# Kernel optimization log

Hardware: AMD Instinct MI355X
Metric: run time of the kernel (lower is better)

## Reference

```python
import jax, jax.numpy as jnp
import numpy as np

N, D, H, E, L = 4096, 512, 8, 131072, 2
DH = D // H  # per-head dim


def _layernorm(x, g, b, eps=1e-5):
    mu = x.mean(-1, keepdims=True)
    v = ((x - mu) ** 2).mean(-1, keepdims=True)
    return (x - mu) * jax.lax.rsqrt(v + eps) * g + b


def setup_inputs() -> dict:
    key = jax.random.key(0)
    ks = jax.random.split(key, 8)
    s = np.float32(1.0 / np.sqrt(D))
    return {
        "x": jax.random.normal(ks[0], (N, D), jnp.float32),
        "edge_index": jax.random.randint(ks[1], (2, E), 0, N),
        "edge_attr": jax.random.normal(ks[2], (E, 16), jnp.float32),
        "W_gcn": jax.random.normal(ks[3], (L, D, D), jnp.float32) * s,
        "ln1_g": jnp.ones((L, D), jnp.float32),
        "ln1_b": jnp.zeros((L, D), jnp.float32),
        "Wq": jax.random.normal(ks[4], (L, D, D), jnp.float32) * s,
        "bq": jnp.zeros((L, D), jnp.float32),
        "Wk": jax.random.normal(ks[5], (L, D, D), jnp.float32) * s,
        "bk": jnp.zeros((L, D), jnp.float32),
        "Wv": jax.random.normal(ks[6], (L, D, D), jnp.float32) * s,
        "bv": jnp.zeros((L, D), jnp.float32),
        "Wo": jax.random.normal(ks[7], (L, D, D), jnp.float32) * s,
        "bo": jnp.zeros((L, D), jnp.float32),
        "ln2_g": jnp.ones((L, D), jnp.float32),
        "ln2_b": jnp.zeros((L, D), jnp.float32),
    }


def reference(x, edge_index, edge_attr, W_gcn, ln1_g, ln1_b, Wq, bq, Wk, bk, Wv, bv, Wo, bo, ln2_g, ln2_b):
    src, dst = edge_index[0], edge_index[1]
    # symmetric GCN normalization (add_self_loops=False): deg from scattering 1s at target
    deg = jax.ops.segment_sum(jnp.ones(src.shape[0], x.dtype), dst, num_segments=N)
    dinv = jnp.where(deg > 0, jax.lax.rsqrt(jnp.maximum(deg, 1e-12)), 0.0)
    enorm = (dinv[src] * dinv[dst])[:, None]  # [E,1]
    scale = 1.0 / np.sqrt(D)  # MHA scale = 1/sqrt(D_x), applied to BOTH Q and K
    for i in range(L):
        # GCNConv (no bias): gather - linear - scatter-sum
        h = x @ W_gcn[i]
        h = jax.ops.segment_sum(h[src] * enorm, dst, num_segments=N)
        # PairNorm (scale=1, scale_individually=False)
        c = h - h.mean(0, keepdims=True)
        h = c * jax.lax.rsqrt(1e-5 + (c * c).sum(-1).mean())
        # residual: relu(x) + x
        h = jax.nn.relu(h) + h
        # LayerNorm 1
        h = _layernorm(h, ln1_g[i], ln1_b[i])
        # MultiHeadAttentionBlock (self-attn, B=1) -- faithful raw reshapes of original
        Q = (h @ Wq[i].T + bq[i]) * scale            # [N,D]
        K = (h @ Wk[i].T + bk[i]) * scale            # [N,D]
        V = h @ Wv[i].T + bv[i]                      # [N,D]
        Qr = Q.reshape(H, DH, N).transpose(0, 2, 1)  # view(B*H,d,L).transpose(1,2)
        Kr = K.reshape(H, DH, N)                     # view(B*H,d,L)
        w = jax.nn.softmax(jnp.einsum('hld,hdm->hlm', Qr, Kr), axis=-1)  # [H,N,N]
        Vr = V.reshape(H, DH, N).transpose(0, 2, 1)  # [H,N,d]
        a = jnp.einsum('hlm,hmd->hld', w, Vr).reshape(N, D)
        h = a @ Wo[i].T + bo[i]
        # LayerNorm 2
        x = _layernorm(h, ln2_g[i], ln2_b[i])
    return x
```

## Files before the change

### kernel.cpp

```cpp
#include <hip/hip_runtime.h>


#define NN 4096
#define DD 512
#define HH 8
#define DH 64
#define EE 131072

typedef float f32x2 __attribute__((ext_vector_type(2)));
typedef float f32x4 __attribute__((ext_vector_type(4)));
typedef short short8 __attribute__((ext_vector_type(8)));
typedef unsigned short u16x4 __attribute__((ext_vector_type(4)));
typedef __bf16 bf16x8 __attribute__((ext_vector_type(8)));

static __device__ __forceinline__ unsigned short f2bf(float f) {
  unsigned u = __float_as_uint(f);
  return (unsigned short)((u + 0x7FFFu + ((u >> 16) & 1u)) >> 16);
}
static __device__ __forceinline__ float bf2f(unsigned short s) {
  return __uint_as_float(((unsigned)s) << 16);
}

static __device__ __forceinline__ f32x4 mfma16(short8 a, short8 b, f32x4 c) {
  return __builtin_amdgcn_mfma_f32_16x16x32_bf16(
      __builtin_bit_cast(bf16x8, a), __builtin_bit_cast(bf16x8, b), c, 0, 0, 0);
}

static __device__ __forceinline__ void gload16(const unsigned short* g, unsigned short* l) {
  __builtin_amdgcn_global_load_lds((const __attribute__((address_space(1))) unsigned int*)g,
                                   (__attribute__((address_space(3))) unsigned int*)l, 16, 0, 0);
}

__global__ __launch_bounds__(256) void deg_k(const int* __restrict__ ei, float* __restrict__ deg) {
  int t = blockIdx.x * 256 + threadIdx.x;
  atomicAdd(&deg[ei[EE + t]], 1.0f);
}

__global__ __launch_bounds__(256) void dinv_k(const float* __restrict__ deg, float* __restrict__ dinv) {
  int t = blockIdx.x * 256 + threadIdx.x;
  float dg = deg[t];
  dinv[t] = dg > 0.f ? rsqrtf(fmaxf(dg, 1e-12f)) : 0.f;
}

__global__ __launch_bounds__(256) void scan_k(const float* __restrict__ deg,
                                              int* __restrict__ rowstart,
                                              int* __restrict__ cursor) {
  __shared__ int part[256];
  const int t = threadIdx.x;
  int loc[16];
  int s = 0;
#pragma unroll
  for (int j = 0; j < 16; ++j) {
    loc[j] = s;
    s += (int)deg[t * 16 + j];
  }
  part[t] = s;
  __syncthreads();
  for (int off = 1; off < 256; off <<= 1) {
    int v = (t >= off) ? part[t - off] : 0;
    __syncthreads();
    part[t] += v;
    __syncthreads();
  }
  int base = (t > 0) ? part[t - 1] : 0;
#pragma unroll
  for (int j = 0; j < 16; ++j) {
    int rs = base + loc[j];
    rowstart[t * 16 + j] = rs;
    cursor[t * 16 + j] = rs;
  }
  if (t == 255) rowstart[4096] = part[255];
}

__global__ __launch_bounds__(256) void csr_fill_k(const int* __restrict__ ei,
                                                  const float* __restrict__ dinv,
                                                  int* __restrict__ cursor,
                                                  int* __restrict__ ecol,
                                                  float* __restrict__ ewt) {
  int e = blockIdx.x * 256 + threadIdx.x;
  int s = ei[e], d = ei[EE + e];
  int pos = atomicAdd(&cursor[d], 1);
  ecol[pos] = s;
  ewt[pos] = dinv[s] * dinv[d];
}

__global__ __launch_bounds__(256) void cvt_k(const float* __restrict__ s,
                                             unsigned short* __restrict__ d, int n4) {
  int i = blockIdx.x * 256 + threadIdx.x;
  if (i < n4) {
    f32x4 v = *(const f32x4*)&s[i * 4];
    u16x4 o;
#pragma unroll
    for (int j = 0; j < 4; ++j) o[j] = f2bf(v[j]);
    *(u16x4*)&d[i * 4] = o;
  }
}

__global__ __launch_bounds__(256) void wtr_k(const float* __restrict__ in,
                                             unsigned short* __restrict__ out) {
  __shared__ unsigned short sm[64][72];
  const int k0 = blockIdx.y * 64, j0 = blockIdx.x * 64;
  const int t = threadIdx.x;
  const int r = t >> 2, q = (t & 3) * 16;
  const float* src = in + (size_t)(k0 + r) * 512 + j0 + q;
#pragma unroll
  for (int jj = 0; jj < 16; ++jj) sm[r][q + jj] = f2bf(src[jj]);
  __syncthreads();
  short8 s0, s1;
#pragma unroll
  for (int j = 0; j < 8; ++j) {
    s0[j] = (short)sm[q + j][r];
    s1[j] = (short)sm[q + 8 + j][r];
  }
  *(short8*)&out[(size_t)(j0 + r) * 512 + k0 + q] = s0;
  *(short8*)&out[(size_t)(j0 + r) * 512 + k0 + q + 8] = s1;
}

__global__ __launch_bounds__(256) void gather_k(const unsigned short* __restrict__ hb,
                                                const int* __restrict__ rowstart,
                                                const int* __restrict__ ecol,
                                                const float* __restrict__ ewt,
                                                float* __restrict__ h1) {
  __shared__ int s_col[256];
  __shared__ float s_w[256];
  const int node = blockIdx.x, t = threadIdx.x;
  const int beg = rowstart[node], end = rowstart[node + 1];
  float a0 = 0.f, a1 = 0.f;
  for (int base = beg; base < end; base += 256) {
    int n = min(256, end - base);
    __syncthreads();
    if (t < n) {
      s_col[t] = ecol[base + t];
      s_w[t] = ewt[base + t];
    }
    __syncthreads();
    for (int j = 0; j < n; ++j) {
      int s = s_col[j];
      float en = s_w[j];
      unsigned v = *(const unsigned*)&hb[(size_t)s * DD + 2 * t];
      a0 += en * __uint_as_float(v << 16);
      a1 += en * __uint_as_float(v & 0xFFFF0000u);
    }
  }
  f32x2 acc = {a0, a1};
  *(f32x2*)&h1[(size_t)node * DD + 2 * t] = acc;
}

template <bool HAS_BIAS, bool OUT_BF16>
__global__ __launch_bounds__(256) void gemm_bt_k(const unsigned short* __restrict__ A,
                                                 const unsigned short* __restrict__ B,
                                                 const float* __restrict__ bias, float scale,
                                                 void* __restrict__ Cv, int M, int Nc, int K) {
  __shared__ __align__(16) unsigned short a_sm[2][64][64];
  __shared__ __align__(16) unsigned short b_sm[2][64][64];
  const int tid = threadIdx.x, w = tid >> 6, lane = tid & 63;
  const int g = lane >> 4, c16 = lane & 15;
  const int n0 = blockIdx.x * 64, m0 = blockIdx.y * 64;
  const int wm = (w >> 1) * 32, wn = (w & 1) * 32;
  const int srow = lane >> 3, cg = lane & 7;
  const int swz = ((cg * 16) ^ (srow << 4)) >> 1;
  const unsigned short* ag = A + (size_t)(m0 + w * 8 + srow) * K + swz;
  const unsigned short* bg = B + (size_t)(n0 + w * 8 + srow) * K + swz;
  f32x4 acc[2][2] = {};

  gload16(ag, &a_sm[0][w * 8][0]);
  gload16(ag + (size_t)32 * K, &a_sm[0][w * 8 + 32][0]);
  gload16(bg, &b_sm[0][w * 8][0]);
  gload16(bg + (size_t)32 * K, &b_sm[0][w * 8 + 32][0]);
  __syncthreads();

  const int rx = (c16 & 7) << 4;
  const int NK = K >> 6;
  for (int ks = 0; ks < NK; ++ks) {
    const int cb = ks & 1;
    if (ks < NK - 1) {
      const size_t ko = (size_t)(ks + 1) * 64;
      gload16(ag + ko, &a_sm[cb ^ 1][w * 8][0]);
      gload16(ag + ko + (size_t)32 * K, &a_sm[cb ^ 1][w * 8 + 32][0]);
      gload16(bg + ko, &b_sm[cb ^ 1][w * 8][0]);
      gload16(bg + ko + (size_t)32 * K, &b_sm[cb ^ 1][w * 8 + 32][0]);
    }
#pragma unroll
    for (int kc = 0; kc < 2; ++kc) {
      const int co = (kc * 64 + g * 16) ^ rx;
      short8 af0 = *(const short8*)((const char*)&a_sm[cb][wm + c16][0] + co);
      short8 af1 = *(const short8*)((const char*)&a_sm[cb][wm + 16 + c16][0] + co);
      short8 bf0 = *(const short8*)((const char*)&b_sm[cb][wn + c16][0] + co);
      short8 bf1 = *(const short8*)((const char*)&b_sm[cb][wn + 16 + c16][0] + co);
      acc[0][0] = mfma16(af0, bf0, acc[0][0]);
      acc[0][1] = mfma16(af0, bf1, acc[0][1]);
      acc[1][0] = mfma16(af1, bf0, acc[1][0]);
      acc[1][1] = mfma16(af1, bf1, acc[1][1]);
    }
    __syncthreads();
  }
#pragma unroll
  for (int fm = 0; fm < 2; ++fm)
#pragma unroll
    for (int fn = 0; fn < 2; ++fn)
#pragma unroll
      for (int r = 0; r < 4; ++r) {
        int row = m0 + wm + fm * 16 + g * 4 + r;
        int col = n0 + wn + fn * 16 + c16;
        float v = acc[fm][fn][r];
        if (HAS_BIAS) v += bias[col];
        v *= scale;
        if (OUT_BF16)
          ((unsigned short*)Cv)[(size_t)row * Nc + col] = f2bf(v);
        else
          ((float*)Cv)[(size_t)row * Nc + col] = v;
      }
}

__global__ __launch_bounds__(256) void colstat_k(const float* __restrict__ hin,
                                                 float* __restrict__ colsum,
                                                 float* __restrict__ sumsq) {
  const int t = threadIdx.x;
  const int r0 = blockIdx.x * 32;
  float a0 = 0.f, a1 = 0.f, sq = 0.f;
  for (int r = 0; r < 32; ++r) {
    float v0 = hin[(size_t)(r0 + r) * DD + t];
    float v1 = hin[(size_t)(r0 + r) * DD + 256 + t];
    a0 += v0; a1 += v1;
    sq += v0 * v0 + v1 * v1;
  }
  atomicAdd(&colsum[t], a0);
  atomicAdd(&colsum[t + 256], a1);
#pragma unroll
  for (int m = 1; m <= 32; m <<= 1) sq += __shfl_xor(sq, m);
  __shared__ float rr[4];
  int w = t >> 6, lane = t & 63;
  if (lane == 0) rr[w] = sq;
  __syncthreads();
  if (t == 0) atomicAdd(sumsq, rr[0] + rr[1] + rr[2] + rr[3]);
}

__global__ __launch_bounds__(256) void finalize_pn_k(const float* __restrict__ colsum,
                                                     const float* __restrict__ sumsq,
                                                     float* __restrict__ mu,
                                                     float* __restrict__ rnp) {
  const int t = threadIdx.x;
  float m0 = colsum[t] * (1.f / (float)NN);
  float m1 = colsum[t + 256] * (1.f / (float)NN);
  mu[t] = m0;
  mu[t + 256] = m1;
  float sq = m0 * m0 + m1 * m1;
#pragma unroll
  for (int m = 1; m <= 32; m <<= 1) sq += __shfl_xor(sq, m);
  __shared__ float rr[4];
  int w = t >> 6, lane = t & 63;
  if (lane == 0) rr[w] = sq;
  __syncthreads();
  if (t == 0) {
    float musq = rr[0] + rr[1] + rr[2] + rr[3];
    *rnp = rsqrtf(1e-5f + (*sumsq) * (1.f / (float)NN) - musq);
  }
}

template <bool PN, bool WF32>
__global__ __launch_bounds__(256) void rowfuse_k(const float* __restrict__ hin,
                                                 const float* __restrict__ mu,
                                                 const float* __restrict__ rnp,
                                                 const float* __restrict__ gg,
                                                 const float* __restrict__ bb,
                                                 float* __restrict__ outf,
                                                 unsigned short* __restrict__ outb) {
  const int row = blockIdx.x, t = threadIdx.x;
  const size_t base = (size_t)row * DD;
  f32x2 vv = *(const f32x2*)&hin[base + 2 * t];
  float v0 = vv[0], v1 = vv[1];
  if (PN) {
    float rn = *rnp;
    v0 = (v0 - mu[2 * t]) * rn;
    v1 = (v1 - mu[2 * t + 1]) * rn;
    v0 = fmaxf(v0, 0.f) + v0;
    v1 = fmaxf(v1, 0.f) + v1;
  }
  float s1 = v0 + v1, s2 = v0 * v0 + v1 * v1;
#pragma unroll
  for (int m = 1; m <= 32; m <<= 1) {
    s1 += __shfl_xor(s1, m);
    s2 += __shfl_xor(s2, m);
  }
  __shared__ float r1[4], r2[4];
  int w = t >> 6, lane = t & 63;
  if (lane == 0) { r1[w] = s1; r2[w] = s2; }
  __syncthreads();
  s1 = r1[0] + r1[1] + r1[2] + r1[3];
  s2 = r2[0] + r2[1] + r2[2] + r2[3];
  float mean = s1 * (1.f / (float)DD);
  float var = s2 * (1.f / (float)DD) - mean * mean;
  float inv = rsqrtf(var + 1e-5f);
  float y0 = (v0 - mean) * inv * gg[2 * t] + bb[2 * t];
  float y1 = (v1 - mean) * inv * gg[2 * t + 1] + bb[2 * t + 1];
  if (WF32) {
    f32x2 yo = {y0, y1};
    *(f32x2*)&outf[base + 2 * t] = yo;
  }
  *(unsigned*)&outb[base + 2 * t] = (unsigned)f2bf(y0) | ((unsigned)f2bf(y1) << 16);
}

__global__ __launch_bounds__(256) void transpose_pk(const unsigned short* __restrict__ in,
                                                    unsigned short* __restrict__ out) {
  __shared__ __align__(16) unsigned short sm[64][72];
  const int m0 = blockIdx.x * 64, p0 = blockIdx.y * 64;
  const int t = threadIdx.x;
  const int r = t >> 2, q = (t & 3) * 16;
  *(short8*)&sm[r][q] = *(const short8*)&in[(size_t)(p0 + r) * NN + m0 + q];
  *(short8*)&sm[r][q + 8] = *(const short8*)&in[(size_t)(p0 + r) * NN + m0 + q + 8];
  __syncthreads();
  short8 s0, s1;
#pragma unroll
  for (int j = 0; j < 8; ++j) {
    s0[j] = (short)sm[q + j][r];
    s1[j] = (short)sm[q + 8 + j][r];
  }
  *(short8*)&out[(size_t)(m0 + r) * DD + p0 + q] = s0;
  *(short8*)&out[(size_t)(m0 + r) * DD + p0 + q + 8] = s1;
}

__global__ __launch_bounds__(256, 4) void attn_k(const unsigned short* __restrict__ Qt,
                                                 const unsigned short* __restrict__ Kt,
                                                 const unsigned short* __restrict__ Vb,
                                                 unsigned short* __restrict__ Op0,
                                                 unsigned short* __restrict__ Op1,
                                                 float* __restrict__ ms) {
  __shared__ __align__(16) unsigned short k_sm[2][64][64];
  __shared__ __align__(16) unsigned short v_sm[2][64][64];
  __shared__ __align__(16) unsigned short p_sm[4][16][64];
  const int tid = threadIdx.x, w = tid >> 6, lane = tid & 63;
  const int g = lane >> 4, c16 = lane & 15;
  const int h = blockIdx.y, z = blockIdx.z;
  const int zbase = z * (NN / 2);
  const int l0 = blockIdx.x * 64 + w * 16;
  unsigned short* __restrict__ Op = z ? Op1 : Op0;

  short8 qf0 = *(const short8*)&Qt[(size_t)(l0 + c16) * DD + h * 64 + g * 8];
  short8 qf1 = *(const short8*)&Qt[(size_t)(l0 + c16) * DD + h * 64 + 32 + g * 8];

  const int srow = lane >> 3, cg = lane & 7;
  const int swz = ((cg * 16) ^ (srow << 4)) >> 1;
  const unsigned short* kgbase = Kt + (size_t)(zbase + w * 16 + srow) * DD + h * 64 + swz;
  const unsigned short* vgbase = Vb + (size_t)(h * 64 + w * 16 + srow) * NN + zbase + swz;

  gload16(kgbase, &k_sm[0][w * 16][0]);
  gload16(kgbase + (size_t)8 * DD, &k_sm[0][w * 16 + 8][0]);
  gload16(vgbase, &v_sm[0][w * 16][0]);
  gload16(vgbase + (size_t)8 * NN, &v_sm[0][w * 16 + 8][0]);
  __syncthreads();

  float M = 0.f;
  f32x4 sacc = {};
  f32x4 oacc[4] = {};
  const int sx = (c16 & 7) << 4;
  short8 ones8;
#pragma unroll
  for (int j = 0; j < 8; ++j) ones8[j] = (short)0x3F80;

  for (int t = 0; t < 32; ++t) {
    const int cb = t & 1;
    if (t < 31) {
      const size_t ko = (size_t)(t + 1) * 64 * DD;
      gload16(kgbase + ko, &k_sm[cb ^ 1][w * 16][0]);
      gload16(kgbase + ko + (size_t)8 * DD, &k_sm[cb ^ 1][w * 16 + 8][0]);
      gload16(vgbase + (t + 1) * 64, &v_sm[cb ^ 1][w * 16][0]);
      gload16(vgbase + (t + 1) * 64 + (size_t)8 * NN, &v_sm[cb ^ 1][w * 16 + 8][0]);
    }
    f32x4 sf[4] = {};
#pragma unroll
    for (int fn = 0; fn < 4; ++fn) {
      const char* kr = (const char*)&k_sm[cb][fn * 16 + c16][0];
      short8 b0 = *(const short8*)(kr + ((g * 16) ^ sx));
      short8 b1 = *(const short8*)(kr + ((64 + g * 16) ^ sx));
      sf[fn] = mfma16(qf0, b0, sf[fn]);
      sf[fn] = mfma16(qf1, b1, sf[fn]);
    }
    float a0 = fmaxf(fmaxf(sf[0][0], sf[0][1]), fmaxf(sf[0][2], sf[0][3]));
    float a1 = fmaxf(fmaxf(sf[1][0], sf[1][1]), fmaxf(sf[1][2], sf[1][3]));
    float a2 = fmaxf(fmaxf(sf[2][0], sf[2][1]), fmaxf(sf[2][2], sf[2][3]));
    float a3 = fmaxf(fmaxf(sf[3][0], sf[3][1]), fmaxf(sf[3][2], sf[3][3]));
    float amax = fmaxf(fmaxf(a0, a1), fmaxf(a2, a3));
    if (__any(amax > M + 25.f)) {
      float wmax = amax;
#pragma unroll
      for (int m = 1; m <= 32; m <<= 1) wmax = fmaxf(wmax, __shfl_xor(wmax, m));
      float alpha = __expf(M - wmax);
#pragma unroll
      for (int r = 0; r < 4; ++r) sacc[r] *= alpha;
#pragma unroll
      for (int fd = 0; fd < 4; ++fd)
#pragma unroll
        for (int r = 0; r < 4; ++r) oacc[fd][r] *= alpha;
      M = wmax;
    }
#pragma unroll
    for (int fn = 0; fn < 4; ++fn)
#pragma unroll
      for (int r = 0; r < 4; ++r) sf[fn][r] = __expf(sf[fn][r] - M);
#pragma unroll
    for (int fn = 0; fn < 4; ++fn)
#pragma unroll
      for (int r = 0; r < 4; ++r) p_sm[w][g * 4 + r][fn * 16 + c16] = f2bf(sf[fn][r]);
#pragma unroll
    for (int kk = 0; kk < 2; ++kk) {
      short8 pa = *(const short8*)&p_sm[w][c16][kk * 32 + g * 8];
      sacc = mfma16(pa, ones8, sacc);
#pragma unroll
      for (int fd = 0; fd < 4; ++fd) {
        const char* vr = (const char*)&v_sm[cb][fd * 16 + c16][0];
        short8 vbf = *(const short8*)(vr + ((kk * 64 + g * 16) ^ sx));
        oacc[fd] = mfma16(pa, vbf, oacc[fd]);
      }
    }
    __syncthreads();
  }
#pragma unroll
  for (int fd = 0; fd < 4; ++fd)
#pragma unroll
    for (int r = 0; r < 4; ++r) {
      int l = l0 + g * 4 + r;
      Op[((size_t)h * NN + l) * DH + fd * 16 + c16] = f2bf(oacc[fd][r]);
    }
  if (c16 == 0) {
#pragma unroll
    for (int r = 0; r < 4; ++r) {
      int hl = h * NN + l0 + g * 4 + r;
      f32x2 pr = {M, sacc[r]};
      *(f32x2*)&ms[((size_t)z * (HH * NN) + hl) * 2] = pr;
    }
  }
}

__global__ __launch_bounds__(256) void attn_merge_k(const unsigned short* __restrict__ Op0,
                                                    const unsigned short* __restrict__ Op1,
                                                    const float* __restrict__ ms,
                                                    unsigned short* __restrict__ Out) {
  const int t = threadIdx.x;
  const int hl = blockIdx.x * 4 + (t >> 6);
  const int d = t & 63;
  float M0 = ms[(size_t)hl * 2], s0 = ms[(size_t)hl * 2 + 1];
  float M1 = ms[((size_t)(HH * NN) + hl) * 2], s1 = ms[((size_t)(HH * NN) + hl) * 2 + 1];
  float M = fmaxf(M0, M1);
  float w0 = __expf(M0 - M), w1 = __expf(M1 - M);
  float inv = 1.f / (w0 * s0 + w1 * s1);
  size_t idx = (size_t)hl * DH + d;
  Out[idx] = f2bf((w0 * bf2f(Op0[idx]) + w1 * bf2f(Op1[idx])) * inv);
}

extern "C" void kernel_launch(void* const* d_in, const int* in_sizes, int n_in,
                              void* d_out, int out_size, void* d_ws, size_t ws_size,
                              hipStream_t stream) {
  const float* x = (const float*)d_in[0];
  const int* ei = (const int*)d_in[1];
  const float* Wg = (const float*)d_in[3];
  const float* ln1g = (const float*)d_in[4];
  const float* ln1b = (const float*)d_in[5];
  const float* Wq = (const float*)d_in[6];
  const float* bq = (const float*)d_in[7];
  const float* Wk = (const float*)d_in[8];
  const float* bk = (const float*)d_in[9];
  const float* Wv = (const float*)d_in[10];
  const float* bv = (const float*)d_in[11];
  const float* Wo = (const float*)d_in[12];
  const float* bo = (const float*)d_in[13];
  const float* ln2g = (const float*)d_in[14];
  const float* ln2b = (const float*)d_in[15];
  float* out = (float*)d_out;

  char* p = (char*)d_ws;
  float* deg = (float*)p;
  float* dinv = deg + 4096;
  float* colsum = deg + 8192;
  float* sumsq = deg + 8704;
  float* mu = deg + 8768;
  float* rnp = deg + 9280;
  float* h1 = deg + 16384;
  unsigned short* xb = (unsigned short*)(h1 + (1u << 21));
  unsigned short* actb = xb + (1u << 21);
  unsigned short* h4b = actb + (1u << 21);
  unsigned short* proj = h4b + (1u << 21);
  unsigned short* Vb = proj + (1u << 21);
  unsigned short* Qt = Vb + (1u << 21);
  unsigned short* Kt = Qt + (1u << 21);
  unsigned short* wb = Kt + (1u << 21);
  float* msbuf = (float*)(wb + 10u * 262144);
  int* rowstart = (int*)(msbuf + 131072);
  int* cursor = rowstart + 4104;
  int* ecol = cursor + 4096;
  float* ewt = (float*)(ecol + EE);
  const size_t needed = (size_t)((char*)(ewt + EE) - (char*)d_ws);
  if (ws_size < needed) return;

  unsigned short* Op0b = (unsigned short*)h1;
  unsigned short* Op1b = h4b;

  const float SCALE = 0.044194173824159216f;
  const size_t WS = (size_t)DD * DD;
  const int W4 = 65536;

  hipMemsetAsync(deg, 0, 4096 * sizeof(float), stream);
  deg_k<<<EE / 256, 256, 0, stream>>>(ei, deg);
  dinv_k<<<NN / 256, 256, 0, stream>>>(deg, dinv);
  scan_k<<<1, 256, 0, stream>>>(deg, rowstart, cursor);
  csr_fill_k<<<EE / 256, 256, 0, stream>>>(ei, dinv, cursor, ecol, ewt);

  cvt_k<<<2048, 256, 0, stream>>>(x, xb, 524288);
  for (int i = 0; i < 2; ++i) {
    wtr_k<<<dim3(8, 8), 256, 0, stream>>>(Wg + i * WS, wb + (0 + i) * 262144);
    cvt_k<<<256, 256, 0, stream>>>(Wq + i * WS, wb + (2 + i) * 262144, W4);
    cvt_k<<<256, 256, 0, stream>>>(Wk + i * WS, wb + (4 + i) * 262144, W4);
    cvt_k<<<256, 256, 0, stream>>>(Wv + i * WS, wb + (6 + i) * 262144, W4);
    cvt_k<<<256, 256, 0, stream>>>(Wo + i * WS, wb + (8 + i) * 262144, W4);
  }

  const dim3 gg(8, 64);
  for (int i = 0; i < 2; ++i) {
    gemm_bt_k<false, true><<<gg, 256, 0, stream>>>(
        xb, wb + (0 + i) * 262144, nullptr, 1.f, actb, NN, DD, DD);
    gather_k<<<NN, 256, 0, stream>>>(actb, rowstart, ecol, ewt, h1);
    hipMemsetAsync(colsum, 0, 513 * sizeof(float), stream);
    colstat_k<<<128, 256, 0, stream>>>(h1, colsum, sumsq);
    finalize_pn_k<<<1, 256, 0, stream>>>(colsum, sumsq, mu, rnp);
    rowfuse_k<true, false><<<NN, 256, 0, stream>>>(h1, mu, rnp, ln1g + i * DD, ln1b + i * DD,
                                                   nullptr, h4b);
    gemm_bt_k<true, true><<<gg, 256, 0, stream>>>(
        h4b, wb + (2 + i) * 262144, bq + i * DD, SCALE, proj, NN, DD, DD);
    transpose_pk<<<dim3(64, 8), 256, 0, stream>>>(proj, Qt);
    gemm_bt_k<true, true><<<gg, 256, 0, stream>>>(
        h4b, wb + (4 + i) * 262144, bk + i * DD, SCALE, proj, NN, DD, DD);
    transpose_pk<<<dim3(64, 8), 256, 0, stream>>>(proj, Kt);
    gemm_bt_k<true, true><<<gg, 256, 0, stream>>>(
        h4b, wb + (6 + i) * 262144, bv + i * DD, 1.f, Vb, NN, DD, DD);
    attn_k<<<dim3(64, 8, 2), 256, 0, stream>>>(Qt, Kt, Vb, Op0b, Op1b, msbuf);
    attn_merge_k<<<HH * NN / 4, 256, 0, stream>>>(Op0b, Op1b, msbuf, actb);
    gemm_bt_k<true, false><<<gg, 256, 0, stream>>>(
        actb, wb + (8 + i) * 262144, bo + i * DD, 1.f, h1, NN, DD, DD);
    rowfuse_k<false, true><<<NN, 256, 0, stream>>>(h1, nullptr, nullptr, ln2g + i * DD,
                                                   ln2b + i * DD, out, xb);
  }
}
```

Before: 457.7 us.

## Batch weight conversions, merge Q/K transposes, swizzle P smem, use hardware bf16 cvt

Replaces the per-layer weight conversion launches with one batched transpose kernel and one 8-way conversion kernel. The Q and K transposes are merged into a single launch, with K now written to the actb buffer so both transposes can run together. The attention P tile in shared memory gets an XOR swizzle to reduce bank conflicts. f2bf switches to the compiler's native bf16 conversion instead of manual rounding. Together these aim to cut launch overhead and LDS conflicts, at some risk of changed NaN rounding behaviour and buffer aliasing mistakes.

```diff
diff --git a/kernel.cpp b/kernel.cpp
--- a/kernel.cpp
+++ b/kernel.cpp
@@ -14,8 +14,7 @@
 typedef __bf16 bf16x8 __attribute__((ext_vector_type(8)));
 
 static __device__ __forceinline__ unsigned short f2bf(float f) {
-  unsigned u = __float_as_uint(f);
-  return (unsigned short)((u + 0x7FFFu + ((u >> 16) & 1u)) >> 16);
+  return __builtin_bit_cast(unsigned short, (__bf16)f);
 }
 static __device__ __forceinline__ float bf2f(unsigned short s) {
   return __uint_as_float(((unsigned)s) << 16);
@@ -96,13 +95,29 @@
   }
 }
 
-__global__ __launch_bounds__(256) void wtr_k(const float* __restrict__ in,
-                                             unsigned short* __restrict__ out) {
+struct P8 { const float* p[8]; };
+__global__ __launch_bounds__(256) void cvt8_k(P8 s, unsigned short* __restrict__ d) {
+  const int which = blockIdx.y;
+  const float* src = s.p[which];
+  unsigned short* dst = d + (size_t)which * 262144;
+  int i = blockIdx.x * 256 + threadIdx.x;
+  f32x4 v = *(const f32x4*)&src[i * 4];
+  u16x4 o;
+#pragma unroll
+  for (int j = 0; j < 4; ++j) o[j] = f2bf(v[j]);
+  *(u16x4*)&dst[i * 4] = o;
+}
+
+__global__ __launch_bounds__(256) void wtr2_k(const float* __restrict__ in,
+                                              unsigned short* __restrict__ out) {
   __shared__ unsigned short sm[64][72];
+  const int z = blockIdx.z;
+  const float* inz = in + (size_t)z * DD * DD;
+  unsigned short* outz = out + (size_t)z * 262144;
   const int k0 = blockIdx.y * 64, j0 = blockIdx.x * 64;
   const int t = threadIdx.x;
   const int r = t >> 2, q = (t & 3) * 16;
-  const float* src = in + (size_t)(k0 + r) * 512 + j0 + q;
+  const float* src = inz + (size_t)(k0 + r) * 512 + j0 + q;
 #pragma unroll
   for (int jj = 0; jj < 16; ++jj) sm[r][q + jj] = f2bf(src[jj]);
   __syncthreads();
@@ -112,8 +127,8 @@
     s0[j] = (short)sm[q + j][r];
     s1[j] = (short)sm[q + 8 + j][r];
   }
-  *(short8*)&out[(size_t)(j0 + r) * 512 + k0 + q] = s0;
-  *(short8*)&out[(size_t)(j0 + r) * 512 + k0 + q + 8] = s1;
+  *(short8*)&outz[(size_t)(j0 + r) * 512 + k0 + q] = s0;
+  *(short8*)&outz[(size_t)(j0 + r) * 512 + k0 + q + 8] = s1;
 }
 
 __global__ __launch_bounds__(256) void gather_k(const unsigned short* __restrict__ hb,
@@ -300,9 +315,13 @@
   *(unsigned*)&outb[base + 2 * t] = (unsigned)f2bf(y0) | ((unsigned)f2bf(y1) << 16);
 }
 
-__global__ __launch_bounds__(256) void transpose_pk(const unsigned short* __restrict__ in,
-                                                    unsigned short* __restrict__ out) {
+__global__ __launch_bounds__(256) void transpose2_pk(const unsigned short* __restrict__ in0,
+                                                     const unsigned short* __restrict__ in1,
+                                                     unsigned short* __restrict__ out0,
+                                                     unsigned short* __restrict__ out1) {
   __shared__ __align__(16) unsigned short sm[64][72];
+  const unsigned short* in = blockIdx.z ? in1 : in0;
+  unsigned short* out = blockIdx.z ? out1 : out0;
   const int m0 = blockIdx.x * 64, p0 = blockIdx.y * 64;
   const int t = threadIdx.x;
   const int r = t >> 2, q = (t & 3) * 16;
@@ -400,10 +419,15 @@
 #pragma unroll
     for (int fn = 0; fn < 4; ++fn)
 #pragma unroll
-      for (int r = 0; r < 4; ++r) p_sm[w][g * 4 + r][fn * 16 + c16] = f2bf(sf[fn][r]);
+      for (int r = 0; r < 4; ++r) {
+        const int prow = g * 4 + r;
+        const int pb = ((fn * 16 + c16) * 2) ^ ((prow & 7) << 4);
+        *(unsigned short*)((char*)&p_sm[w][prow][0] + pb) = f2bf(sf[fn][r]);
+      }
 #pragma unroll
     for (int kk = 0; kk < 2; ++kk) {
-      short8 pa = *(const short8*)&p_sm[w][c16][kk * 32 + g * 8];
+      const int rb = (kk * 64 + g * 16) ^ ((c16 & 7) << 4);
+      short8 pa = *(const short8*)((const char*)&p_sm[w][c16][0] + rb);
       sacc = mfma16(pa, ones8, sacc);
 #pragma unroll
       for (int fd = 0; fd < 4; ++fd) {
@@ -496,7 +520,6 @@
 
   const float SCALE = 0.044194173824159216f;
   const size_t WS = (size_t)DD * DD;
-  const int W4 = 65536;
 
   hipMemsetAsync(deg, 0, 4096 * sizeof(float), stream);
   deg_k<<<EE / 256, 256, 0, stream>>>(ei, deg);
@@ -505,13 +528,13 @@
   csr_fill_k<<<EE / 256, 256, 0, stream>>>(ei, dinv, cursor, ecol, ewt);
 
   cvt_k<<<2048, 256, 0, stream>>>(x, xb, 524288);
-  for (int i = 0; i < 2; ++i) {
-    wtr_k<<<dim3(8, 8), 256, 0, stream>>>(Wg + i * WS, wb + (0 + i) * 262144);
-    cvt_k<<<256, 256, 0, stream>>>(Wq + i * WS, wb + (2 + i) * 262144, W4);
-    cvt_k<<<256, 256, 0, stream>>>(Wk + i * WS, wb + (4 + i) * 262144, W4);
-    cvt_k<<<256, 256, 0, stream>>>(Wv + i * WS, wb + (6 + i) * 262144, W4);
-    cvt_k<<<256, 256, 0, stream>>>(Wo + i * WS, wb + (8 + i) * 262144, W4);
-  }
+  wtr2_k<<<dim3(8, 8, 2), 256, 0, stream>>>(Wg, wb);
+  P8 s8;
+  s8.p[0] = Wq; s8.p[1] = Wq + WS;
+  s8.p[2] = Wk; s8.p[3] = Wk + WS;
+  s8.p[4] = Wv; s8.p[5] = Wv + WS;
+  s8.p[6] = Wo; s8.p[7] = Wo + WS;
+  cvt8_k<<<dim3(256, 8), 256, 0, stream>>>(s8, wb + 2u * 262144);
 
   const dim3 gg(8, 64);
   for (int i = 0; i < 2; ++i) {
@@ -525,12 +548,11 @@
                                                    nullptr, h4b);
     gemm_bt_k<true, true><<<gg, 256, 0, stream>>>(
         h4b, wb + (2 + i) * 262144, bq + i * DD, SCALE, proj, NN, DD, DD);
-    transpose_pk<<<dim3(64, 8), 256, 0, stream>>>(proj, Qt);
     gemm_bt_k<true, true><<<gg, 256, 0, stream>>>(
-        h4b, wb + (4 + i) * 262144, bk + i * DD, SCALE, proj, NN, DD, DD);
-    transpose_pk<<<dim3(64, 8), 256, 0, stream>>>(proj, Kt);
+        h4b, wb + (4 + i) * 262144, bk + i * DD, SCALE, actb, NN, DD, DD);
     gemm_bt_k<true, true><<<gg, 256, 0, stream>>>(
         h4b, wb + (6 + i) * 262144, bv + i * DD, 1.f, Vb, NN, DD, DD);
+    transpose2_pk<<<dim3(64, 8, 2), 256, 0, stream>>>(proj, actb, Qt, Kt);
     attn_k<<<dim3(64, 8, 2), 256, 0, stream>>>(Qt, Kt, Vb, Op0b, Op1b, msbuf);
     attn_merge_k<<<HH * NN / 4, 256, 0, stream>>>(Op0b, Op1b, msbuf, actb);
     gemm_bt_k<true, false><<<gg, 256, 0, stream>>>(
```

Measured after the change: 432.3 us. -5.6%, faster.
